# Optimization experiments

Hardware: AMD Instinct MI355X
Metric: run time of the kernel (lower is better)

Reference implementation:

```python
import jax, jax.numpy as jnp
import numpy as np

L_MAX = 3
N_RADIAL = [2, 2, 1, 1]  # radial powers r^{2k} with 2k+l <= l_max=3


def fibonacci_sphere(n):
    i = np.arange(n, dtype=np.float64)
    phi = np.pi * (3.0 - np.sqrt(5.0))
    y = 1.0 - 2.0 * i / (n - 1)
    r = np.sqrt(np.maximum(1.0 - y * y, 0.0))
    th = phi * i
    pts = np.stack([np.cos(th) * r, y, np.sin(th) * r], -1)
    return jnp.asarray(pts, dtype=jnp.float32)


def real_sh(u):
    # real spherical harmonics on unit vectors u[...,3], degrees 0..3
    x, y, z = u[..., 0], u[..., 1], u[..., 2]
    Y0 = 0.28209479 * jnp.ones_like(x)[..., None]
    Y1 = 0.48860251 * jnp.stack([y, z, x], -1)
    Y2 = jnp.stack([
        1.09254843 * x * y,
        1.09254843 * y * z,
        0.31539157 * (3.0 * z * z - 1.0),
        1.09254843 * x * z,
        0.54627421 * (x * x - y * y)], -1)
    Y3 = jnp.stack([
        0.59004359 * y * (3.0 * x * x - y * y),
        2.89061144 * x * y * z,
        0.45704579 * y * (5.0 * z * z - 1.0),
        0.37317633 * z * (5.0 * z * z - 3.0),
        0.45704579 * x * (5.0 * z * z - 1.0),
        1.44530572 * z * (x * x - y * y),
        0.59004359 * x * (x * x - 3.0 * y * y)], -1)
    return [Y0, Y1, Y2, Y3]


def grid_sample_3d(vol, grid):
    # vol: [B, D, H, W]; grid: [B, d, h, w, 3], grid[...,0]->W, [...,1]->H, [...,2]->D
    # align_corners=True, zeros padding (torch.nn.functional.grid_sample semantics)
    B, Dv, Hv, Wv = vol.shape
    ix = (grid[..., 0] + 1.0) * 0.5 * (Wv - 1)
    iy = (grid[..., 1] + 1.0) * 0.5 * (Hv - 1)
    iz = (grid[..., 2] + 1.0) * 0.5 * (Dv - 1)
    x0f, y0f, z0f = jnp.floor(ix), jnp.floor(iy), jnp.floor(iz)
    wx, wy, wz = ix - x0f, iy - y0f, iz - z0f
    x0, y0, z0 = x0f.astype(jnp.int32), y0f.astype(jnp.int32), z0f.astype(jnp.int32)
    x1, y1, z1 = x0 + 1, y0 + 1, z0 + 1
    bidx = jnp.arange(B).reshape(B, 1, 1, 1)

    def tap(zi, yi, xi):
        m = ((zi >= 0) & (zi < Dv) & (yi >= 0) & (yi < Hv) & (xi >= 0) & (xi < Wv)).astype(vol.dtype)
        v = vol[bidx, jnp.clip(zi, 0, Dv - 1), jnp.clip(yi, 0, Hv - 1), jnp.clip(xi, 0, Wv - 1)]
        return v * m

    out = (tap(z0, y0, x0) * (1 - wz) * (1 - wy) * (1 - wx)
         + tap(z0, y0, x1) * (1 - wz) * (1 - wy) * wx
         + tap(z0, y1, x0) * (1 - wz) * wy * (1 - wx)
         + tap(z0, y1, x1) * (1 - wz) * wy * wx
         + tap(z1, y0, x0) * wz * (1 - wy) * (1 - wx)
         + tap(z1, y0, x1) * wz * (1 - wy) * wx
         + tap(z1, y1, x0) * wz * wy * (1 - wx)
         + tap(z1, y1, x1) * wz * wy * wx)
    return out


def setup_inputs() -> dict:
    key = jax.random.key(0)
    ks = jax.random.split(key, 12)
    B, H, W, D, S = 8, 32, 32, 32, 64
    x = jax.random.normal(ks[0], (B, H, W, D, 3), jnp.float32) * 0.35
    x_density = jax.random.uniform(ks[1], (B, H, W, D), jnp.float32)
    F = jax.random.normal(ks[2], (B, S, 256), jnp.float32) * 0.1
    def lin(k, i, o):
        return jax.random.normal(k, (i, o), jnp.float32) / np.sqrt(i)
    return {
        'x': x, 'x_density': x_density, 'F': F,
        'S2': fibonacci_sphere(S),
        'bw1': lin(ks[3], 256, 64), 'bb1': jnp.zeros((64,), jnp.float32),
        'bw2': lin(ks[4], 64, 3), 'bb2': jnp.zeros((3,), jnp.float32),
        'cw1': lin(ks[5], 256, 128), 'cb1': jnp.zeros((128,), jnp.float32),
        'cw2': lin(ks[6], 128, 64), 'cb2': jnp.zeros((64,), jnp.float32),
        'iw': lin(ks[7], 128, 3), 'ib': jnp.zeros((3,), jnp.float32),
    }


def reference(x, x_density, F, S2, bw1, bb1, bw2, bb2, cw1, cb1, cw2, cb2, iw, ib):
    B, H, W, D, _ = x.shape
    S = S2.shape[0]
    quad = (4.0 * jnp.pi) / S  # sphere quadrature weight for fibonacci samples
    Ybase = real_sh(S2)  # list of [S, 2l+1]

    # frame (E) branch: basis MLP -> type-1 SH coefficients -> normalize
    basis = jax.nn.relu(F @ bw1 + bb1) @ bw2 + bb2          # [B,S,3]
    E = jnp.einsum('vm,bvc->bmc', Ybase[1], basis) * quad   # [B,3,3]
    E = E / jnp.clip(jnp.linalg.norm(E, axis=-1, keepdims=True), 1e-6)

    # latent code branch: code MLP -> full SHT coefficients per degree l
    latent = jax.nn.relu(F @ cw1 + cb1) @ cw2 + cb2         # [B,S,64]
    coeffs = [jnp.einsum('vm,bvc->bmc', Ybase[l], latent) * quad for l in range(L_MAX + 1)]

    # zernike monomials of the grid points
    xf = x.reshape(B, -1, 3)                                # [B,V,3]
    r = jnp.linalg.norm(xf, axis=-1, keepdims=True)         # [B,V,1]
    u = xf / jnp.clip(r, 1e-6)
    Yx = real_sh(u)
    points_code = []
    points_inv = None
    for l in range(L_MAX + 1):
        Pl = Yx[l] * (r ** l)                               # solid harmonic [B,V,2l+1]
        rad = jnp.stack([r[..., 0] ** (2 * k) for k in range(N_RADIAL[l])], -1)  # [B,V,n_l]
        zl = Pl[..., :, None] * rad[..., None, :]           # [B,V,2l+1,n_l]
        p = jnp.einsum('bmi,bvmj->bvij', coeffs[l], zl)     # [B,V,64,n_l]
        p = p.reshape(B, p.shape[1], -1)
        points_code.append(p)
        if l == 1:
            points_inv = p                                  # [B,V,128]
    points_code = jnp.concatenate(points_code, -1)          # [B,V,384]

    pts = points_inv @ iw + ib                              # [B,V,3]
    coords = pts.reshape(B, H, W, D, 3)
    vol = x_density.reshape(B, H, W, D)
    sampled = grid_sample_3d(vol, coords)                   # [B,H,W,D]
    return sampled, E, coords, points_code
```

## Files before the change

kernel.cpp:

```cpp
#include <hip/hip_runtime.h>
#include <math.h>

#define OFF_E     262144
#define OFF_COORD 262216
#define OFF_CODE  1048648

#define QUAD 0.19634954084936207f

#define WS_H1 0
#define WS_H2 32768
#define WS_C  98304
#define WS_AB 106496

__global__ __launch_bounds__(256) void k_hidden(
    const float* __restrict__ F,
    const float* __restrict__ bw1, const float* __restrict__ bb1,
    const float* __restrict__ cw1, const float* __restrict__ cb1,
    float* __restrict__ ws)
{
    __shared__ float sF[8 * 256];
    const int blk = blockIdx.x;
    const int b   = blk >> 3;
    const int r0  = (blk & 7) * 8;
    const int tid = threadIdx.x;

    float* wsH1 = ws + WS_H1;
    float* wsH2 = ws + WS_H2;

    const float* Fb = F + ((size_t)b * 64 + r0) * 256;
    for (int i = tid; i < 2048; i += 256) sF[i] = Fb[i];
    __syncthreads();

    for (int e = tid; e < 512; e += 256) {
        const int v = e >> 6, k = e & 63;
        const float* fr = sF + v * 256;
        float acc = bb1[k];
        #pragma unroll 8
        for (int j = 0; j < 256; ++j) acc = fmaf(fr[j], bw1[j * 64 + k], acc);
        wsH1[((size_t)b * 64 + r0 + v) * 64 + k] = fmaxf(acc, 0.f);
    }
    for (int e = tid; e < 1024; e += 256) {
        const int v = e >> 7, k = e & 127;
        const float* fr = sF + v * 256;
        float acc = cb1[k];
        #pragma unroll 8
        for (int j = 0; j < 256; ++j) acc = fmaf(fr[j], cw1[j * 128 + k], acc);
        wsH2[((size_t)b * 64 + r0 + v) * 128 + k] = fmaxf(acc, 0.f);
    }
}

__global__ __launch_bounds__(512) void k_coeffs(
    const float* __restrict__ ws_in,
    const float* __restrict__ S2,
    const float* __restrict__ bw2, const float* __restrict__ bb2,
    const float* __restrict__ cw2, const float* __restrict__ cb2,
    const float* __restrict__ iw,
    float* __restrict__ ws_out, float* __restrict__ outE)
{
    __shared__ float sH2[64 * 128];
    __shared__ float sLat[64 * 64];
    __shared__ float sY[64 * 16];
    __shared__ float sBas[64 * 3];
    __shared__ float sC[16 * 64];
    __shared__ float sE[9];

    const int b = blockIdx.x, tid = threadIdx.x;
    const float* wsH1 = ws_in + WS_H1;
    const float* wsH2 = ws_in + WS_H2;
    float* wsC  = ws_out + WS_C;
    float* wsAB = ws_out + WS_AB;

    const float* H2b = wsH2 + (size_t)b * 8192;
    for (int i = tid; i < 8192; i += 512) sH2[i] = H2b[i];

    if (tid < 64) {
        const float x = S2[tid * 3 + 0], y = S2[tid * 3 + 1], z = S2[tid * 3 + 2];
        float* Yv = sY + tid * 16;
        Yv[0]  = 0.28209479f;
        Yv[1]  = 0.48860251f * y;
        Yv[2]  = 0.48860251f * z;
        Yv[3]  = 0.48860251f * x;
        Yv[4]  = 1.09254843f * x * y;
        Yv[5]  = 1.09254843f * y * z;
        Yv[6]  = 0.31539157f * (3.f * z * z - 1.f);
        Yv[7]  = 1.09254843f * x * z;
        Yv[8]  = 0.54627421f * (x * x - y * y);
        Yv[9]  = 0.59004359f * y * (3.f * x * x - y * y);
        Yv[10] = 2.89061144f * x * y * z;
        Yv[11] = 0.45704579f * y * (5.f * z * z - 1.f);
        Yv[12] = 0.37317633f * z * (5.f * z * z - 3.f);
        Yv[13] = 0.45704579f * x * (5.f * z * z - 1.f);
        Yv[14] = 1.44530572f * z * (x * x - y * y);
        Yv[15] = 0.59004359f * x * (x * x - 3.f * y * y);
    }

    float breg = 0.f;
    if (tid < 192) {
        const int v = tid / 3, c = tid % 3;
        const float* h1 = wsH1 + ((size_t)b * 64 + v) * 64;
        float acc = bb2[c];
        #pragma unroll 8
        for (int k = 0; k < 64; ++k) acc = fmaf(h1[k], bw2[k * 3 + c], acc);
        breg = acc;
    }
    __syncthreads();

    if (tid < 192) sBas[tid] = breg;

    for (int e = tid; e < 4096; e += 512) {
        const int v = e >> 6, i = e & 63;
        const float* h2 = sH2 + v * 128;
        float acc = cb2[i];
        #pragma unroll 8
        for (int k = 0; k < 128; ++k) acc = fmaf(h2[k], cw2[k * 64 + i], acc);
        sLat[e] = acc;
    }
    __syncthreads();

    for (int o = tid; o < 1024; o += 512) {
        const int m = o >> 6, i = o & 63;
        float acc = 0.f;
        #pragma unroll 8
        for (int v = 0; v < 64; ++v) acc = fmaf(sY[v * 16 + m], sLat[v * 64 + i], acc);
        acc *= QUAD;
        sC[o] = acc;
        wsC[(size_t)b * 1024 + o] = acc;
    }
    if (tid < 9) {
        const int m = tid / 3, c = tid % 3;
        float acc = 0.f;
        for (int v = 0; v < 64; ++v) acc = fmaf(sY[v * 16 + 1 + m], sBas[v * 3 + c], acc);
        sE[tid] = acc * QUAD;
    }
    __syncthreads();

    if (tid < 9) {
        const int m = tid / 3;
        const float e0 = sE[m * 3 + 0], e1 = sE[m * 3 + 1], e2 = sE[m * 3 + 2];
        const float n = sqrtf(e0 * e0 + e1 * e1 + e2 * e2);
        outE[b * 9 + tid] = sE[tid] / fmaxf(n, 1e-6f);
    }
    if (tid < 18) {
        const int which = tid / 9, mc = tid % 9;
        const int m = mc / 3, c = mc % 3;
        float acc = 0.f;
        #pragma unroll 8
        for (int i = 0; i < 64; ++i)
            acc = fmaf(sC[(1 + m) * 64 + i], iw[(2 * i + which) * 3 + c], acc);
        wsAB[b * 18 + tid] = acc;
    }
}

template <int NM, int MOFF, bool HASJ>
__device__ __forceinline__ void phaseC(const float* __restrict__ sC,
                                       const float* __restrict__ sZ,
                                       float* __restrict__ out,
                                       size_t base, int i, int j)
{
    float cr[NM];
    #pragma unroll
    for (int m = 0; m < NM; ++m) cr[m] = sC[(MOFF + m) * 64 + i];
    #pragma unroll 4
    for (int v = 0; v < 64; ++v) {
        const float* Z = sZ + v * 17;
        float acc = 0.f;
        #pragma unroll
        for (int m = 0; m < NM; ++m) acc = fmaf(cr[m], Z[MOFF + m], acc);
        if (HASJ && j) acc *= Z[16];
        out[base + (size_t)v * 384] = acc;
    }
}

__global__ __launch_bounds__(384) void k_points(
    const float* __restrict__ x, const float* __restrict__ dens,
    const float* __restrict__ ws, const float* __restrict__ ib,
    float* __restrict__ out)
{
    __shared__ float sC[16 * 64];
    __shared__ float sAB[18];
    __shared__ float sZ[64 * 17];

    const int blk = blockIdx.x;
    const int b   = blk >> 9;
    const int v0  = (blk & 511) * 64;
    const int tid = threadIdx.x;

    const float* wsC  = ws + WS_C;
    const float* wsAB = ws + WS_AB;

    for (int i = tid; i < 1024; i += 384) sC[i] = wsC[(size_t)b * 1024 + i];
    if (tid < 18) sAB[tid] = wsAB[b * 18 + tid];

    if (tid < 64) {
        const int v = v0 + tid;
        const size_t g = (size_t)b * 32768 + v;
        const float px = x[g * 3 + 0], py = x[g * 3 + 1], pz = x[g * 3 + 2];
        const float r2 = px * px + py * py + pz * pz;
        const float r  = sqrtf(r2);
        const float inv = 1.f / fmaxf(r, 1e-6f);
        const float ux = px * inv, uy = py * inv, uz = pz * inv;
        float* Z = sZ + tid * 17;
        Z[0] = 0.28209479f;
        Z[1] = 0.48860251f * uy * r;
        Z[2] = 0.48860251f * uz * r;
        Z[3] = 0.48860251f * ux * r;
        Z[4] = 1.09254843f * ux * uy * r2;
        Z[5] = 1.09254843f * uy * uz * r2;
        Z[6] = 0.31539157f * (3.f * uz * uz - 1.f) * r2;
        Z[7] = 1.09254843f * ux * uz * r2;
        Z[8] = 0.54627421f * (ux * ux - uy * uy) * r2;
        const float r3 = r2 * r;
        Z[9]  = 0.59004359f * uy * (3.f * ux * ux - uy * uy) * r3;
        Z[10] = 2.89061144f * ux * uy * uz * r3;
        Z[11] = 0.45704579f * uy * (5.f * uz * uz - 1.f) * r3;
        Z[12] = 0.37317633f * uz * (5.f * uz * uz - 3.f) * r3;
        Z[13] = 0.45704579f * ux * (5.f * uz * uz - 1.f) * r3;
        Z[14] = 1.44530572f * uz * (ux * ux - uy * uy) * r3;
        Z[15] = 0.59004359f * ux * (ux * ux - 3.f * uy * uy) * r3;
        Z[16] = r2;

        float pt[3];
        #pragma unroll
        for (int c = 0; c < 3; ++c) {
            float acc = ib[c];
            #pragma unroll
            for (int m = 0; m < 3; ++m)
                acc += Z[1 + m] * (sAB[m * 3 + c] + r2 * sAB[9 + m * 3 + c]);
            pt[c] = acc;
            out[OFF_COORD + g * 3 + c] = acc;
        }

        const float ix = (pt[0] + 1.f) * 0.5f * 31.f;
        const float iy = (pt[1] + 1.f) * 0.5f * 31.f;
        const float iz = (pt[2] + 1.f) * 0.5f * 31.f;
        const float x0f = floorf(ix), y0f = floorf(iy), z0f = floorf(iz);
        const float wx = ix - x0f, wy = iy - y0f, wz = iz - z0f;
        const int x0 = (int)x0f, y0 = (int)y0f, z0 = (int)z0f;
        const float* volb = dens + (size_t)b * 32768;
        float s = 0.f;
        #pragma unroll
        for (int dz = 0; dz < 2; ++dz) {
            const int zi = z0 + dz;
            const float wzz = dz ? wz : 1.f - wz;
            #pragma unroll
            for (int dy = 0; dy < 2; ++dy) {
                const int yi = y0 + dy;
                const float wyy = dy ? wy : 1.f - wy;
                #pragma unroll
                for (int dx = 0; dx < 2; ++dx) {
                    const int xi = x0 + dx;
                    const float wxx = dx ? wx : 1.f - wx;
                    if (zi >= 0 && zi < 32 && yi >= 0 && yi < 32 && xi >= 0 && xi < 32)
                        s += wzz * wyy * wxx * volb[zi * 1024 + yi * 32 + xi];
                }
            }
        }
        out[g] = s;
    }
    __syncthreads();

    const int c = tid;
    const size_t base = OFF_CODE + ((size_t)b * 32768 + v0) * 384 + c;
    if (c < 128) {
        phaseC<1, 0, true>(sC, sZ, out, base, c >> 1, c & 1);
    } else if (c < 256) {
        const int cc = c - 128;
        phaseC<3, 1, true>(sC, sZ, out, base, cc >> 1, cc & 1);
    } else if (c < 320) {
        phaseC<5, 4, false>(sC, sZ, out, base, c - 256, 0);
    } else {
        phaseC<7, 9, false>(sC, sZ, out, base, c - 320, 0);
    }
}

extern "C" void kernel_launch(void* const* d_in, const int* in_sizes, int n_in,
                              void* d_out, int out_size, void* d_ws, size_t ws_size,
                              hipStream_t stream) {
    const float* x    = (const float*)d_in[0];
    const float* dens = (const float*)d_in[1];
    const float* F    = (const float*)d_in[2];
    const float* S2   = (const float*)d_in[3];
    const float* bw1  = (const float*)d_in[4];
    const float* bb1  = (const float*)d_in[5];
    const float* bw2  = (const float*)d_in[6];
    const float* bb2  = (const float*)d_in[7];
    const float* cw1  = (const float*)d_in[8];
    const float* cb1  = (const float*)d_in[9];
    const float* cw2  = (const float*)d_in[10];
    const float* cb2  = (const float*)d_in[11];
    const float* iw   = (const float*)d_in[12];
    const float* ib   = (const float*)d_in[13];
    float* out = (float*)d_out;
    float* ws  = (float*)d_ws;

    k_hidden<<<64, 256, 0, stream>>>(F, bw1, bb1, cw1, cb1, ws);
    k_coeffs<<<8, 512, 0, stream>>>(ws, S2, bw2, bb2, cw2, cb2, iw, ws, out + OFF_E);
    k_points<<<4096, 384, 0, stream>>>(x, dens, ws, ib, out);
}
```

Before: 576.0 us.

## Vectorize points_code output with float4 nontemporal stores and per-thread column quads

Changes how the 384-wide points_code tile is written. Each thread now computes four adjacent output columns for 16 voxels and writes them with one float4 nontemporal store, where before each thread wrote one scalar column across all 64 voxels. The l=0 term folds in the Y0 constant directly, and each row is written in full 128-bit transactions that bypass cache retention. The cost is more registers per thread for the l=2 and l=3 coefficient blocks, and the work per thread is uneven across the four branches.

Result: slower. 598.1 us (+3.8%).

```diff
diff --git a/kernel.cpp b/kernel.cpp
--- a/kernel.cpp
+++ b/kernel.cpp
@@ -11,6 +11,8 @@
 #define WS_H2 32768
 #define WS_C  98304
 #define WS_AB 106496
+
+typedef __attribute__((ext_vector_type(4))) float f4;
 
 __global__ __launch_bounds__(256) void k_hidden(
     const float* __restrict__ F,
@@ -148,26 +150,6 @@
         for (int i = 0; i < 64; ++i)
             acc = fmaf(sC[(1 + m) * 64 + i], iw[(2 * i + which) * 3 + c], acc);
         wsAB[b * 18 + tid] = acc;
-    }
-}
-
-template <int NM, int MOFF, bool HASJ>
-__device__ __forceinline__ void phaseC(const float* __restrict__ sC,
-                                       const float* __restrict__ sZ,
-                                       float* __restrict__ out,
-                                       size_t base, int i, int j)
-{
-    float cr[NM];
-    #pragma unroll
-    for (int m = 0; m < NM; ++m) cr[m] = sC[(MOFF + m) * 64 + i];
-    #pragma unroll 4
-    for (int v = 0; v < 64; ++v) {
-        const float* Z = sZ + v * 17;
-        float acc = 0.f;
-        #pragma unroll
-        for (int m = 0; m < NM; ++m) acc = fmaf(cr[m], Z[MOFF + m], acc);
-        if (HASJ && j) acc *= Z[16];
-        out[base + (size_t)v * 384] = acc;
     }
 }
 
@@ -259,17 +241,92 @@
     }
     __syncthreads();
 
-    const int c = tid;
-    const size_t base = OFF_CODE + ((size_t)b * 32768 + v0) * 384 + c;
-    if (c < 128) {
-        phaseC<1, 0, true>(sC, sZ, out, base, c >> 1, c & 1);
-    } else if (c < 256) {
-        const int cc = c - 128;
-        phaseC<3, 1, true>(sC, sZ, out, base, cc >> 1, cc & 1);
-    } else if (c < 320) {
-        phaseC<5, 4, false>(sC, sZ, out, base, c - 256, 0);
+    const int q  = tid % 96;
+    const int vg = tid / 96;
+    f4* outq = (f4*)(out + OFF_CODE + ((size_t)b * 32768 + v0) * 384);
+
+    if (q < 32) {
+        const float k0 = 0.28209479f * sC[2 * q];
+        const float k1 = 0.28209479f * sC[2 * q + 1];
+        #pragma unroll 4
+        for (int t = 0; t < 16; ++t) {
+            const int v = vg * 16 + t;
+            const float r2 = sZ[v * 17 + 16];
+            f4 o; o.x = k0; o.y = k0 * r2; o.z = k1; o.w = k1 * r2;
+            __builtin_nontemporal_store(o, outq + (size_t)v * 96 + q);
+        }
+    } else if (q < 64) {
+        const int i0 = 2 * (q - 32);
+        float c0[3], c1[3];
+        #pragma unroll
+        for (int m = 0; m < 3; ++m) {
+            c0[m] = sC[(1 + m) * 64 + i0];
+            c1[m] = sC[(1 + m) * 64 + i0 + 1];
+        }
+        #pragma unroll 4
+        for (int t = 0; t < 16; ++t) {
+            const int v = vg * 16 + t;
+            const float* Z = sZ + v * 17;
+            const float z1 = Z[1], z2 = Z[2], z3 = Z[3], r2 = Z[16];
+            const float a0 = fmaf(c0[0], z1, fmaf(c0[1], z2, c0[2] * z3));
+            const float a1 = fmaf(c1[0], z1, fmaf(c1[1], z2, c1[2] * z3));
+            f4 o; o.x = a0; o.y = a0 * r2; o.z = a1; o.w = a1 * r2;
+            __builtin_nontemporal_store(o, outq + (size_t)v * 96 + q);
+        }
+    } else if (q < 80) {
+        const int i0 = 4 * (q - 64);
+        float cc[4][5];
+        #pragma unroll
+        for (int k = 0; k < 4; ++k)
+            #pragma unroll
+            for (int m = 0; m < 5; ++m)
+                cc[k][m] = sC[(4 + m) * 64 + i0 + k];
+        #pragma unroll 2
+        for (int t = 0; t < 16; ++t) {
+            const int v = vg * 16 + t;
+            const float* Z = sZ + v * 17;
+            float z[5];
+            #pragma unroll
+            for (int m = 0; m < 5; ++m) z[m] = Z[4 + m];
+            f4 o;
+            float a[4];
+            #pragma unroll
+            for (int k = 0; k < 4; ++k) {
+                float acc = cc[k][0] * z[0];
+                #pragma unroll
+                for (int m = 1; m < 5; ++m) acc = fmaf(cc[k][m], z[m], acc);
+                a[k] = acc;
+            }
+            o.x = a[0]; o.y = a[1]; o.z = a[2]; o.w = a[3];
+            __builtin_nontemporal_store(o, outq + (size_t)v * 96 + q);
+        }
     } else {
-        phaseC<7, 9, false>(sC, sZ, out, base, c - 320, 0);
+        const int i0 = 4 * (q - 80);
+        float cc[4][7];
+        #pragma unroll
+        for (int k = 0; k < 4; ++k)
+            #pragma unroll
+            for (int m = 0; m < 7; ++m)
+                cc[k][m] = sC[(9 + m) * 64 + i0 + k];
+        #pragma unroll 2
+        for (int t = 0; t < 16; ++t) {
+            const int v = vg * 16 + t;
+            const float* Z = sZ + v * 17;
+            float z[7];
+            #pragma unroll
+            for (int m = 0; m < 7; ++m) z[m] = Z[9 + m];
+            f4 o;
+            float a[4];
+            #pragma unroll
+            for (int k = 0; k < 4; ++k) {
+                float acc = cc[k][0] * z[0];
+                #pragma unroll
+                for (int m = 1; m < 7; ++m) acc = fmaf(cc[k][m], z[m], acc);
+                a[k] = acc;
+            }
+            o.x = a[0]; o.y = a[1]; o.z = a[2]; o.w = a[3];
+            __builtin_nontemporal_store(o, outq + (size_t)v * 96 + q);
+        }
     }
 }
 
```
